# Performance work log

Measured on AMD Instinct MI355X. Metric: run time of the kernel, lower is better.

## Reference

```python
import jax, jax.numpy as jnp
import numpy as np

H = 16  # num_heads
D = 64  # head_dim (latent_dim // num_heads)


def setup_inputs() -> dict:
    key = jax.random.key(0)
    ks = jax.random.split(key, 14)
    B, L, S = 2, 1024, 4096
    input_dim, latent_dim, latent_rank = 2048, 1024, 128
    sc = 0.02
    return {
        "latent": jax.random.normal(ks[0], (B, L, latent_dim), jnp.float32),
        "x": jax.random.normal(ks[1], (B, S, input_dim), jnp.float32),
        "Wq": jax.random.normal(ks[2], (latent_dim, latent_dim), jnp.float32) * sc,
        "bq": jnp.zeros((latent_dim,), jnp.float32),
        "Wc": jax.random.normal(ks[3], (input_dim, latent_rank), jnp.float32) * sc,
        "bc": jnp.zeros((latent_rank,), jnp.float32),
        "Wk": jax.random.normal(ks[4], (latent_rank, latent_dim), jnp.float32) * sc,
        "bk": jnp.zeros((latent_dim,), jnp.float32),
        "Wv": jax.random.normal(ks[5], (latent_rank, latent_dim), jnp.float32) * sc,
        "bv": jnp.zeros((latent_dim,), jnp.float32),
        "Wo": jax.random.normal(ks[6], (latent_dim, latent_dim), jnp.float32) * sc,
        "bo": jnp.zeros((latent_dim,), jnp.float32),
    }


def reference(latent, x, Wq, bq, Wc, bc, Wk, bk, Wv, bv, Wo, bo):
    B, L, latent_dim = latent.shape
    S = x.shape[1]
    # projections
    Q = latent @ Wq + bq                      # [B, L, latent_dim]
    compressed = x @ Wc + bc                  # [B, S, latent_rank] low-rank latent
    K_full = compressed @ Wk + bk             # [B, S, latent_dim]
    V_full = compressed @ Wv + bv             # [B, S, latent_dim]
    # split heads -> [B, H, len, D]
    Qh = Q.reshape(B, L, H, D).transpose(0, 2, 1, 3)
    Kh = K_full.reshape(B, S, H, D).transpose(0, 2, 1, 3)
    Vh = V_full.reshape(B, S, H, D).transpose(0, 2, 1, 3)
    scale = 1.0 / jnp.sqrt(jnp.float32(D))
    scores = jnp.einsum("bhld,bhsd->bhls", Qh, Kh) * scale  # [B,H,L,S]
    attn = jax.nn.softmax(scores, axis=-1)
    ctx = jnp.einsum("bhls,bhsd->bhld", attn, Vh)            # [B,H,L,D]
    ctx = ctx.transpose(0, 2, 1, 3).reshape(B, L, latent_dim)
    return ctx @ Wo + bo
```

## Files before the change

### kernel.cpp

```cpp
#include <hip/hip_runtime.h>
#include <hip/hip_bf16.h>

using bf16x8  = __attribute__((ext_vector_type(8))) short;
using ushort8 = __attribute__((ext_vector_type(8))) unsigned short;
using f32x4   = __attribute__((ext_vector_type(4))) float;

#define DEVINL __device__ __forceinline__

DEVINL unsigned short f2bf(float f) {
    unsigned u = __builtin_bit_cast(unsigned, f);
    u += 0x7FFFu + ((u >> 16) & 1u);
    return (unsigned short)(u >> 16);
}

DEVINL void gload_lds16(const void* g, void* l) {
    __builtin_amdgcn_global_load_lds(
        (const __attribute__((address_space(1))) void*)g,
        (__attribute__((address_space(3))) void*)l, 16, 0, 0);
}

__global__ __launch_bounds__(256) void k_convT(const float* __restrict__ i0,
                                               unsigned short* __restrict__ o0,
                                               const float* __restrict__ i1,
                                               unsigned short* __restrict__ o1,
                                               int R, int C) {
    __shared__ float t[32][33];
    const float* in = blockIdx.z ? i1 : i0;
    unsigned short* out = blockIdx.z ? o1 : o0;
    int c0 = blockIdx.x * 32, r0 = blockIdx.y * 32;
    int tx = threadIdx.x, ty = threadIdx.y;
#pragma unroll
    for (int i = 0; i < 4; i++)
        t[ty + i * 8][tx] = in[(size_t)(r0 + ty + i * 8) * C + c0 + tx];
    __syncthreads();
#pragma unroll
    for (int i = 0; i < 4; i++)
        out[(size_t)(c0 + ty + i * 8) * R + r0 + tx] = f2bf(t[tx][ty + i * 8]);
}

template <int BM, int BN, int OUTBF, int BIASROW, int AMODE>
__global__ __launch_bounds__(256) void k_gemm(const void* __restrict__ Ain,
                                              const unsigned short* __restrict__ BT,
                                              const float* __restrict__ bias,
                                              void* __restrict__ Cout,
                                              int M, int N, int K, float scale,
                                              size_t zA, size_t zB, size_t zC,
                                              const float2* __restrict__ ML) {
    constexpr int WM = BM / 2, WN = BN / 2, MI = WM / 16, NI = WN / 16;
    constexpr int CB = BN * 8 / 256;
    constexpr int CA = BM * 8 / 256;
    constexpr int EPT = BM * 64 / 256;
    constexpr int TPR = 64 / EPT;
    constexpr int NAREG = (AMODE == 2) ? EPT / 2 : (AMODE == 1 ? EPT / 4 : 1);
    __shared__ unsigned short ls[2][(BM + BN) * 64];
    const int tid = threadIdx.x, lane = tid & 63, w = tid >> 6;
    const int m0 = blockIdx.y * BM, n0 = blockIdx.x * BN, zz = blockIdx.z;
    const int mw = (w >> 1) * WM, nw = (w & 1) * WN;
    const int r16 = lane & 15, g4 = lane >> 4;
    const unsigned short* A16 = (const unsigned short*)Ain + zA * zz;
    const float* A32 = (const float*)Ain;
    BT += zB * zz;
    const int arow = tid / TPR, acol = (tid % TPR) * EPT;

    float4 areg[NAREG];
    float2 mle[2];

    f32x4 acc[MI][NI];
#pragma unroll
    for (int a = 0; a < MI; a++)
#pragma unroll
        for (int b = 0; b < NI; b++) acc[a][b] = (f32x4){0.f, 0.f, 0.f, 0.f};

    auto LOAD_A = [&](int bufi, int k0) {
        if constexpr (AMODE == 0) {
#pragma unroll
            for (int i = 0; i < CA; i++) {
                int ch = i * 256 + w * 64 + lane;
                int row = ch >> 3, c = ch & 7;
                gload_lds16(A16 + (size_t)(m0 + row) * K + k0 + c * 8,
                            &ls[bufi][(size_t)(i * 256 + w * 64) * 8]);
            }
        } else if constexpr (AMODE == 1) {
            const float* src = A32 + (size_t)(m0 + arow) * K + k0 + acol;
#pragma unroll
            for (int j = 0; j < EPT / 4; j++) areg[j] = *(const float4*)(src + j * 4);
        } else {
            const float* src = A32 + (size_t)(m0 + arow) * K + k0 + acol;
#pragma unroll
            for (int j = 0; j < EPT / 4; j++) {
                areg[j] = *(const float4*)(src + j * 4);
                areg[j + EPT / 4] = *(const float4*)(src + 2097152 + j * 4);
            }
            int b = (m0 + arow) >> 10, q = (m0 + arow) & 1023, h = k0 >> 6;
            mle[0] = ML[((size_t)(b * 16 + h)) * 1024 + q];
            mle[1] = ML[((size_t)((2 + b) * 16 + h)) * 1024 + q];
        }
    };

    auto WRITE_A = [&](int bufi) {
        if constexpr (AMODE == 1) {
            unsigned u[EPT / 2];
#pragma unroll
            for (int j = 0; j < EPT / 4; j++) {
                asm("v_cvt_pk_bf16_f32 %0, %1, %2"
                    : "=v"(u[2 * j]) : "v"(areg[j].x), "v"(areg[j].y));
                asm("v_cvt_pk_bf16_f32 %0, %1, %2"
                    : "=v"(u[2 * j + 1]) : "v"(areg[j].z), "v"(areg[j].w));
            }
#pragma unroll
            for (int j = 0; j < EPT / 8; j++)
                *(uint4*)&ls[bufi][arow * 64 + acol + j * 8] =
                    make_uint4(u[4 * j], u[4 * j + 1], u[4 * j + 2], u[4 * j + 3]);
        } else if constexpr (AMODE == 2) {
            float Mx = fmaxf(mle[0].x, mle[1].x);
            float w0 = exp2f(mle[0].x - Mx), w1 = exp2f(mle[1].x - Mx);
            float inv = 1.f / (w0 * mle[0].y + w1 * mle[1].y);
            w0 *= inv; w1 *= inv;
            unsigned u[EPT / 2];
#pragma unroll
            for (int j = 0; j < EPT / 4; j++) {
                float4 a = areg[j], c = areg[j + EPT / 4];
                float v0 = w0 * a.x + w1 * c.x, v1 = w0 * a.y + w1 * c.y;
                float v2 = w0 * a.z + w1 * c.z, v3 = w0 * a.w + w1 * c.w;
                asm("v_cvt_pk_bf16_f32 %0, %1, %2" : "=v"(u[2 * j]) : "v"(v0), "v"(v1));
                asm("v_cvt_pk_bf16_f32 %0, %1, %2" : "=v"(u[2 * j + 1]) : "v"(v2), "v"(v3));
            }
#pragma unroll
            for (int j = 0; j < EPT / 8; j++)
                *(uint4*)&ls[bufi][arow * 64 + acol + j * 8] =
                    make_uint4(u[4 * j], u[4 * j + 1], u[4 * j + 2], u[4 * j + 3]);
        }
    };

    auto STAGE_B = [&](int bufi, int k0) {
        unsigned short* lsB = &ls[bufi][BM * 64];
#pragma unroll
        for (int i = 0; i < CB; i++) {
            int ch = i * 256 + w * 64 + lane;
            int row = ch >> 3, c = ch & 7;
            gload_lds16(BT + (size_t)(n0 + row) * K + k0 + c * 8,
                        lsB + (size_t)(i * 256 + w * 64) * 8);
        }
    };

    auto COMPUTE = [&](int bufi) {
        const unsigned short* lsA = ls[bufi];
        const unsigned short* lsB = &ls[bufi][BM * 64];
#pragma unroll
        for (int kk = 0; kk < 2; kk++) {
            bf16x8 af[MI], bfr[NI];
#pragma unroll
            for (int a = 0; a < MI; a++)
                af[a] = *(const bf16x8*)&lsA[(mw + a * 16 + r16) * 64 + kk * 32 + g4 * 8];
#pragma unroll
            for (int b = 0; b < NI; b++)
                bfr[b] = *(const bf16x8*)&lsB[(nw + b * 16 + r16) * 64 + kk * 32 + g4 * 8];
#pragma unroll
            for (int a = 0; a < MI; a++)
#pragma unroll
                for (int b = 0; b < NI; b++)
                    acc[a][b] = __builtin_amdgcn_mfma_f32_16x16x32_bf16(af[a], bfr[b], acc[a][b], 0, 0, 0);
        }
    };

    const int nk = K >> 6;
    LOAD_A(0, 0);
    STAGE_B(0, 0);
    if constexpr (AMODE != 0) WRITE_A(0);
    __syncthreads();
    for (int t = 0; t < nk; ++t) {
        int cur = t & 1, nxt = cur ^ 1;
        if (t + 1 < nk) { LOAD_A(nxt, (t + 1) << 6); STAGE_B(nxt, (t + 1) << 6); }
        COMPUTE(cur);
        if (AMODE != 0 && t + 1 < nk) WRITE_A(nxt);
        __syncthreads();
    }

#pragma unroll
    for (int b = 0; b < NI; b++) {
        int col = n0 + nw + b * 16 + r16;
        float bvc = BIASROW ? 0.f : bias[col];
#pragma unroll
        for (int a = 0; a < MI; a++) {
#pragma unroll
            for (int r = 0; r < 4; r++) {
                int row = m0 + mw + a * 16 + g4 * 4 + r;
                float bv = BIASROW ? bias[row] : bvc;
                float v = (acc[a][b][r] + bv) * scale;
                if (OUTBF)
                    ((unsigned short*)Cout)[zC * zz + (size_t)row * N + col] = f2bf(v);
                else
                    ((float*)Cout)[zC * zz + (size_t)row * N + col] = v;
            }
        }
    }
}

__global__ __launch_bounds__(256, 4) void k_attn(const unsigned short* __restrict__ Qb,
                                                 const unsigned short* __restrict__ Kb,
                                                 const unsigned short* __restrict__ VTb,
                                                 float* __restrict__ ctxp,
                                                 float2* __restrict__ ML) {
    constexpr int LD = 1024;
    __shared__ unsigned short lsK[2][64 * 64];
    __shared__ unsigned short lsVT[2][64 * 64];
    __shared__ unsigned short lsP[4][16 * 64];
    const int tid = threadIdx.x, lane = tid & 63, w = tid >> 6;
    const int r16 = lane & 15, g4 = lane >> 4;
    const int wg = blockIdx.x;
    const int xcd = wg & 7, t_ = wg >> 3, qi = t_ & 15, gg = t_ >> 4;
    const int g = gg * 8 + xcd;
    const int bh = g & 31, z = g >> 5;
    const int b = bh >> 4, h = bh & 15;
    const int q0 = qi * 64 + w * 16;

    const size_t qbase = ((size_t)b * 1024 + q0 + r16) * LD + h * 64;
    bf16x8 qa0 = *(const bf16x8*)&Qb[qbase + g4 * 8];
    bf16x8 qa1 = *(const bf16x8*)&Qb[qbase + 32 + g4 * 8];

    f32x4 ctxa[4];
#pragma unroll
    for (int d = 0; d < 4; d++) ctxa[d] = (f32x4){0.f, 0.f, 0.f, 0.f};
    float m_run = -1e30f, l_run = 0.f;

    const int s7 = r16 & 7;
    const int offk0 = r16 * 64 + ((g4 ^ s7) << 3);
    const int offk1 = r16 * 64 + (((g4 + 4) ^ s7) << 3);
    const int pwb = r16 * 64 + (g4 & 1) * 4;
    const int c2 = g4 >> 1;
    const int swn0 = ((0 + c2) ^ s7) << 3, swn1 = ((2 + c2) ^ s7) << 3;
    const int swn2 = ((4 + c2) ^ s7) << 3, swn3 = ((6 + c2) ^ s7) << 3;

    const int lrow = lane >> 3, lcol = lane & 7;
    const int csrc = lcol ^ lrow;
    const unsigned short* gK = Kb + (size_t)b * 4096 * LD + h * 64 +
                               (size_t)(w * 8 + lrow) * LD + csrc * 8;
    const unsigned short* gV = VTb + (size_t)bh * 64 * 4096 +
                               (size_t)(w * 8 + lrow) * 4096 + csrc * 8;

    auto STAGE = [&](int bufi, int s0) {
        gload_lds16(gK + (size_t)s0 * LD, &lsK[bufi][(w * 8) * 64]);
        gload_lds16(gK + (size_t)(s0 + 32) * LD, &lsK[bufi][(32 + w * 8) * 64]);
        gload_lds16(gV + s0, &lsVT[bufi][(w * 8) * 64]);
        gload_lds16(gV + s0 + 32 * 4096, &lsVT[bufi][(32 + w * 8) * 64]);
    };

    auto COMPUTE = [&](int bufi) {
        f32x4 sc[4];
#pragma unroll
        for (int ni = 0; ni < 4; ni++) sc[ni] = (f32x4){0.f, 0.f, 0.f, 0.f};
        __builtin_amdgcn_s_setprio(1);
#pragma unroll
        for (int kk = 0; kk < 2; kk++) {
            bf16x8 qa = kk ? qa1 : qa0;
            int ofk = kk ? offk1 : offk0;
#pragma unroll
            for (int ni = 0; ni < 4; ni++) {
                bf16x8 kf = *(const bf16x8*)&lsK[bufi][ni * 1024 + ofk];
                sc[ni] = __builtin_amdgcn_mfma_f32_16x16x32_bf16(kf, qa, sc[ni], 0, 0, 0);
            }
        }
        __builtin_amdgcn_s_setprio(0);

        float pmax = sc[0][0];
#pragma unroll
        for (int ni = 0; ni < 4; ni++)
#pragma unroll
            for (int r = 0; r < 4; r++)
                if (ni || r) pmax = fmaxf(pmax, sc[ni][r]);
        pmax = fmaxf(pmax, __shfl_xor(pmax, 16));
        pmax = fmaxf(pmax, __shfl_xor(pmax, 32));

        if (!__all(pmax <= m_run + 8.f)) {
            float mn = fmaxf(m_run, pmax);
            float corr = exp2f(m_run - mn);
            m_run = mn;
            l_run *= corr;
            float c4[4];
#pragma unroll
            for (int r = 0; r < 4; r++) c4[r] = __shfl(corr, g4 * 4 + r);
#pragma unroll
            for (int di = 0; di < 4; di++)
#pragma unroll
                for (int r = 0; r < 4; r++) ctxa[di][r] *= c4[r];
        }

        float p[4][4];
        float rs = 0.f;
#pragma unroll
        for (int ni = 0; ni < 4; ni++)
#pragma unroll
            for (int r = 0; r < 4; r++) {
                p[ni][r] = exp2f(sc[ni][r] - m_run);
                rs += p[ni][r];
            }
        rs += __shfl_xor(rs, 16);
        rs += __shfl_xor(rs, 32);
        l_run += rs;

#pragma unroll
        for (int ni = 0; ni < 4; ni++) {
            int sw = ni == 0 ? swn0 : ni == 1 ? swn1 : ni == 2 ? swn2 : swn3;
            unsigned u0, u1;
            asm("v_cvt_pk_bf16_f32 %0, %1, %2" : "=v"(u0) : "v"(p[ni][0]), "v"(p[ni][1]));
            asm("v_cvt_pk_bf16_f32 %0, %1, %2" : "=v"(u1) : "v"(p[ni][2]), "v"(p[ni][3]));
            *(uint2*)&lsP[w][pwb + sw] = make_uint2(u0, u1);
        }

        __builtin_amdgcn_s_setprio(1);
#pragma unroll
        for (int kk = 0; kk < 2; kk++) {
            int ofk = kk ? offk1 : offk0;
            bf16x8 pa = *(const bf16x8*)&lsP[w][ofk];
#pragma unroll
            for (int di = 0; di < 4; di++) {
                bf16x8 vf = *(const bf16x8*)&lsVT[bufi][di * 1024 + ofk];
                ctxa[di] = __builtin_amdgcn_mfma_f32_16x16x32_bf16(pa, vf, ctxa[di], 0, 0, 0);
            }
        }
        __builtin_amdgcn_s_setprio(0);
    };

    const int t0 = z * 32, t1 = t0 + 32;
    STAGE(0, t0 * 64);
    __syncthreads();
#pragma unroll 1
    for (int t = t0; t < t1; ++t) {
        int pb = (t - t0) & 1;
        if (t + 1 < t1) STAGE(pb ^ 1, (t + 1) * 64);
        COMPUTE(pb);
        __syncthreads();
    }

    float* cp = ctxp + ((size_t)z * 2 + b) * 1024 * 1024;
#pragma unroll
    for (int r = 0; r < 4; r++) {
        int q = q0 + g4 * 4 + r;
#pragma unroll
        for (int di = 0; di < 4; di++)
            cp[(size_t)q * 1024 + h * 64 + di * 16 + r16] = ctxa[di][r];
    }
    if (g4 == 0)
        ML[(((size_t)z * 2 + b) * 16 + h) * 1024 + q0 + r16] = make_float2(m_run, l_run);
}

extern "C" void kernel_launch(void* const* d_in, const int* in_sizes, int n_in,
                              void* d_out, int out_size, void* d_ws, size_t ws_size,
                              hipStream_t stream) {
    const float* latent = (const float*)d_in[0];
    const float* x      = (const float*)d_in[1];
    const float* Wq     = (const float*)d_in[2];
    const float* bq     = (const float*)d_in[3];
    const float* Wc     = (const float*)d_in[4];
    const float* bc     = (const float*)d_in[5];
    const float* Wk     = (const float*)d_in[6];
    const float* bk     = (const float*)d_in[7];
    const float* Wv     = (const float*)d_in[8];
    const float* bv     = (const float*)d_in[9];
    const float* Wo     = (const float*)d_in[10];
    const float* bo     = (const float*)d_in[11];
    float* out = (float*)d_out;

    char* ws = (char*)d_ws;
    size_t off = 0;
    auto alloc = [&](size_t shorts) {
        void* p = ws + off;
        off += (shorts * 2 + 255) & ~(size_t)255;
        return (unsigned short*)p;
    };
    unsigned short* WqT  = alloc(1048576);
    unsigned short* WcT  = alloc(262144);
    unsigned short* WkT  = alloc(131072);
    unsigned short* WvT  = alloc(131072);
    unsigned short* WoT  = alloc(1048576);
    unsigned short* comp = alloc(1048576);
    unsigned short* Qb   = alloc(2097152);
    unsigned short* Kb   = alloc(8388608);
    unsigned short* VTb  = alloc(8388608);
    float*          ctxp = (float*)alloc(8388608);
    float2*         MLp  = (float2*)alloc(262144);

    dim3 tb(32, 8);
    k_convT<<<dim3(32, 32, 2), tb, 0, stream>>>(Wq, WqT, Wo, WoT, 1024, 1024);
    k_convT<<<dim3(32, 4, 2), tb, 0, stream>>>(Wk, WkT, Wv, WvT, 128, 1024);
    k_convT<<<dim3(4, 64, 1), tb, 0, stream>>>(Wc, WcT, Wc, WcT, 2048, 128);

    k_gemm<32, 128, 1, 0, 1><<<dim3(1, 256, 1), 256, 0, stream>>>(
        x, WcT, bc, comp, 8192, 128, 2048, 1.f, 0, 0, 0, nullptr);
    k_gemm<64, 64, 1, 0, 1><<<dim3(16, 32, 1), 256, 0, stream>>>(
        latent, WqT, bq, Qb, 2048, 1024, 1024, 0.18033688f, 0, 0, 0, nullptr);
    k_gemm<128, 128, 1, 0, 0><<<dim3(8, 64, 1), 256, 0, stream>>>(
        comp, WkT, bk, Kb, 8192, 1024, 128, 1.f, 0, 0, 0, nullptr);
    k_gemm<64, 64, 1, 1, 0><<<dim3(64, 16, 2), 256, 0, stream>>>(
        WvT, comp, bv, VTb, 1024, 4096, 128, 1.f,
        0, (size_t)4096 * 128, (size_t)16 * 64 * 4096, nullptr);
    k_attn<<<1024, 256, 0, stream>>>(Qb, Kb, VTb, ctxp, MLp);
    k_gemm<64, 64, 0, 0, 2><<<dim3(16, 32, 1), 256, 0, stream>>>(
        ctxp, WoT, bo, out, 2048, 1024, 1024, 1.f, 0, 0, 0, MLp);
}
```

Measured before the change: 300.5 us.

## Software-pipeline attention PV with next QK, merge transposes, retile GEMMs

The attention loop is restructured so the PV MFMAs for the previous tile run after the QK MFMAs of the current tile, with V fragments preloaded into registers. This overlaps softmax latency with matrix work, and the row-sum reduction across lanes is deferred to the end. Separately, the three weight-transpose launches are merged into one kernel, and the compress and K projection GEMMs switch to 64x64 tiles for more blocks. The pipelining raises register pressure through the extra V fragment registers, which could lower occupancy.

```diff
diff --git a/kernel.cpp b/kernel.cpp
--- a/kernel.cpp
+++ b/kernel.cpp
@@ -19,15 +19,23 @@
         (__attribute__((address_space(3))) void*)l, 16, 0, 0);
 }
 
-__global__ __launch_bounds__(256) void k_convT(const float* __restrict__ i0,
-                                               unsigned short* __restrict__ o0,
-                                               const float* __restrict__ i1,
-                                               unsigned short* __restrict__ o1,
-                                               int R, int C) {
+__global__ __launch_bounds__(256) void k_convTall(
+        const float* __restrict__ Wq, const float* __restrict__ Wo,
+        const float* __restrict__ Wk, const float* __restrict__ Wv,
+        const float* __restrict__ Wc,
+        unsigned short* __restrict__ WqT, unsigned short* __restrict__ WoT,
+        unsigned short* __restrict__ WkT, unsigned short* __restrict__ WvT,
+        unsigned short* __restrict__ WcT) {
     __shared__ float t[32][33];
-    const float* in = blockIdx.z ? i1 : i0;
-    unsigned short* out = blockIdx.z ? o1 : o0;
-    int c0 = blockIdx.x * 32, r0 = blockIdx.y * 32;
+    int bx = blockIdx.x;
+    const float* in; unsigned short* out; int R, C, tix;
+    if (bx < 1024)      { in = Wq; out = WqT; R = 1024; C = 1024; tix = bx; }
+    else if (bx < 2048) { in = Wo; out = WoT; R = 1024; C = 1024; tix = bx - 1024; }
+    else if (bx < 2176) { in = Wk; out = WkT; R = 128;  C = 1024; tix = bx - 2048; }
+    else if (bx < 2304) { in = Wv; out = WvT; R = 128;  C = 1024; tix = bx - 2176; }
+    else                { in = Wc; out = WcT; R = 2048; C = 128;  tix = bx - 2304; }
+    int ctiles = C >> 5;
+    int c0 = (tix % ctiles) * 32, r0 = (tix / ctiles) * 32;
     int tx = threadIdx.x, ty = threadIdx.y;
 #pragma unroll
     for (int i = 0; i < 4; i++)
@@ -228,8 +236,8 @@
     const int offk1 = r16 * 64 + (((g4 + 4) ^ s7) << 3);
     const int pwb = r16 * 64 + (g4 & 1) * 4;
     const int c2 = g4 >> 1;
-    const int swn0 = ((0 + c2) ^ s7) << 3, swn1 = ((2 + c2) ^ s7) << 3;
-    const int swn2 = ((4 + c2) ^ s7) << 3, swn3 = ((6 + c2) ^ s7) << 3;
+    const int swn[4] = {((0 + c2) ^ s7) << 3, ((2 + c2) ^ s7) << 3,
+                        ((4 + c2) ^ s7) << 3, ((6 + c2) ^ s7) << 3};
 
     const int lrow = lane >> 3, lcol = lane & 7;
     const int csrc = lcol ^ lrow;
@@ -238,6 +246,8 @@
     const unsigned short* gV = VTb + (size_t)bh * 64 * 4096 +
                                (size_t)(w * 8 + lrow) * 4096 + csrc * 8;
 
+    bf16x8 vfr[8];
+
     auto STAGE = [&](int bufi, int s0) {
         gload_lds16(gK + (size_t)s0 * LD, &lsK[bufi][(w * 8) * 64]);
         gload_lds16(gK + (size_t)(s0 + 32) * LD, &lsK[bufi][(32 + w * 8) * 64]);
@@ -245,10 +255,7 @@
         gload_lds16(gV + s0 + 32 * 4096, &lsVT[bufi][(32 + w * 8) * 64]);
     };
 
-    auto COMPUTE = [&](int bufi) {
-        f32x4 sc[4];
-#pragma unroll
-        for (int ni = 0; ni < 4; ni++) sc[ni] = (f32x4){0.f, 0.f, 0.f, 0.f};
+    auto QK = [&](int bufi, f32x4* sc) {
         __builtin_amdgcn_s_setprio(1);
 #pragma unroll
         for (int kk = 0; kk < 2; kk++) {
@@ -261,16 +268,28 @@
             }
         }
         __builtin_amdgcn_s_setprio(0);
-
-        float pmax = sc[0][0];
-#pragma unroll
-        for (int ni = 0; ni < 4; ni++)
-#pragma unroll
-            for (int r = 0; r < 4; r++)
-                if (ni || r) pmax = fmaxf(pmax, sc[ni][r]);
+    };
+
+    auto PV = [&](bf16x8 pa0, bf16x8 pa1) {
+        __builtin_amdgcn_s_setprio(1);
+#pragma unroll
+        for (int kk = 0; kk < 2; kk++) {
+            bf16x8 pa = kk ? pa1 : pa0;
+#pragma unroll
+            for (int di = 0; di < 4; di++)
+                ctxa[di] = __builtin_amdgcn_mfma_f32_16x16x32_bf16(pa, vfr[kk * 4 + di], ctxa[di], 0, 0, 0);
+        }
+        __builtin_amdgcn_s_setprio(0);
+    };
+
+    auto SOFTMAX = [&](f32x4* sc) {
+        float pmax = fmaxf(fmaxf(fmaxf(sc[0][0], sc[0][1]), fmaxf(sc[0][2], sc[0][3])),
+                           fmaxf(fmaxf(sc[1][0], sc[1][1]), fmaxf(sc[1][2], sc[1][3])));
+        pmax = fmaxf(pmax,
+               fmaxf(fmaxf(fmaxf(sc[2][0], sc[2][1]), fmaxf(sc[2][2], sc[2][3])),
+                     fmaxf(fmaxf(sc[3][0], sc[3][1]), fmaxf(sc[3][2], sc[3][3]))));
         pmax = fmaxf(pmax, __shfl_xor(pmax, 16));
         pmax = fmaxf(pmax, __shfl_xor(pmax, 32));
-
         if (!__all(pmax <= m_run + 8.f)) {
             float mn = fmaxf(m_run, pmax);
             float corr = exp2f(m_run - mn);
@@ -284,53 +303,68 @@
 #pragma unroll
                 for (int r = 0; r < 4; r++) ctxa[di][r] *= c4[r];
         }
-
         float p[4][4];
-        float rs = 0.f;
 #pragma unroll
         for (int ni = 0; ni < 4; ni++)
 #pragma unroll
             for (int r = 0; r < 4; r++) {
                 p[ni][r] = exp2f(sc[ni][r] - m_run);
-                rs += p[ni][r];
-            }
-        rs += __shfl_xor(rs, 16);
-        rs += __shfl_xor(rs, 32);
-        l_run += rs;
-
+                l_run += p[ni][r];
+            }
 #pragma unroll
         for (int ni = 0; ni < 4; ni++) {
-            int sw = ni == 0 ? swn0 : ni == 1 ? swn1 : ni == 2 ? swn2 : swn3;
             unsigned u0, u1;
             asm("v_cvt_pk_bf16_f32 %0, %1, %2" : "=v"(u0) : "v"(p[ni][0]), "v"(p[ni][1]));
             asm("v_cvt_pk_bf16_f32 %0, %1, %2" : "=v"(u1) : "v"(p[ni][2]), "v"(p[ni][3]));
-            *(uint2*)&lsP[w][pwb + sw] = make_uint2(u0, u1);
-        }
-
-        __builtin_amdgcn_s_setprio(1);
+            *(uint2*)&lsP[w][pwb + swn[ni]] = make_uint2(u0, u1);
+        }
+    };
+
+    auto LOADVF = [&](int bufi) {
 #pragma unroll
         for (int kk = 0; kk < 2; kk++) {
             int ofk = kk ? offk1 : offk0;
-            bf16x8 pa = *(const bf16x8*)&lsP[w][ofk];
-#pragma unroll
-            for (int di = 0; di < 4; di++) {
-                bf16x8 vf = *(const bf16x8*)&lsVT[bufi][di * 1024 + ofk];
-                ctxa[di] = __builtin_amdgcn_mfma_f32_16x16x32_bf16(pa, vf, ctxa[di], 0, 0, 0);
-            }
-        }
-        __builtin_amdgcn_s_setprio(0);
+#pragma unroll
+            for (int di = 0; di < 4; di++)
+                vfr[kk * 4 + di] = *(const bf16x8*)&lsVT[bufi][di * 1024 + ofk];
+        }
     };
 
     const int t0 = z * 32, t1 = t0 + 32;
     STAGE(0, t0 * 64);
     __syncthreads();
+    {
+        STAGE(1, (t0 + 1) * 64);
+        f32x4 sc[4];
+#pragma unroll
+        for (int ni = 0; ni < 4; ni++) sc[ni] = (f32x4){0.f, 0.f, 0.f, 0.f};
+        QK(0, sc);
+        SOFTMAX(sc);
+        LOADVF(0);
+        __syncthreads();
+    }
 #pragma unroll 1
-    for (int t = t0; t < t1; ++t) {
-        int pb = (t - t0) & 1;
-        if (t + 1 < t1) STAGE(pb ^ 1, (t + 1) * 64);
-        COMPUTE(pb);
+    for (int t = t0 + 1; t < t1; ++t) {
+        int cur = (t - t0) & 1;
+        bf16x8 pa0 = *(const bf16x8*)&lsP[w][offk0];
+        bf16x8 pa1 = *(const bf16x8*)&lsP[w][offk1];
+        if (t + 1 < t1) STAGE(cur ^ 1, (t + 1) * 64);
+        f32x4 sc[4];
+#pragma unroll
+        for (int ni = 0; ni < 4; ni++) sc[ni] = (f32x4){0.f, 0.f, 0.f, 0.f};
+        QK(cur, sc);
+        PV(pa0, pa1);
+        SOFTMAX(sc);
+        LOADVF(cur);
         __syncthreads();
     }
+    {
+        bf16x8 pa0 = *(const bf16x8*)&lsP[w][offk0];
+        bf16x8 pa1 = *(const bf16x8*)&lsP[w][offk1];
+        PV(pa0, pa1);
+    }
+    l_run += __shfl_xor(l_run, 16);
+    l_run += __shfl_xor(l_run, 32);
 
     float* cp = ctxp + ((size_t)z * 2 + b) * 1024 * 1024;
 #pragma unroll
@@ -380,16 +414,13 @@
     float*          ctxp = (float*)alloc(8388608);
     float2*         MLp  = (float2*)alloc(262144);
 
-    dim3 tb(32, 8);
-    k_convT<<<dim3(32, 32, 2), tb, 0, stream>>>(Wq, WqT, Wo, WoT, 1024, 1024);
-    k_convT<<<dim3(32, 4, 2), tb, 0, stream>>>(Wk, WkT, Wv, WvT, 128, 1024);
-    k_convT<<<dim3(4, 64, 1), tb, 0, stream>>>(Wc, WcT, Wc, WcT, 2048, 128);
-
-    k_gemm<32, 128, 1, 0, 1><<<dim3(1, 256, 1), 256, 0, stream>>>(
+    k_convTall<<<2560, dim3(32, 8), 0, stream>>>(Wq, Wo, Wk, Wv, Wc,
+                                                 WqT, WoT, WkT, WvT, WcT);
+    k_gemm<64, 64, 1, 0, 1><<<dim3(2, 128, 1), 256, 0, stream>>>(
         x, WcT, bc, comp, 8192, 128, 2048, 1.f, 0, 0, 0, nullptr);
     k_gemm<64, 64, 1, 0, 1><<<dim3(16, 32, 1), 256, 0, stream>>>(
         latent, WqT, bq, Qb, 2048, 1024, 1024, 0.18033688f, 0, 0, 0, nullptr);
-    k_gemm<128, 128, 1, 0, 0><<<dim3(8, 64, 1), 256, 0, stream>>>(
+    k_gemm<64, 64, 1, 0, 0><<<dim3(16, 128, 1), 256, 0, stream>>>(
         comp, WkT, bk, Kb, 8192, 1024, 128, 1.f, 0, 0, 0, nullptr);
     k_gemm<64, 64, 1, 1, 0><<<dim3(64, 16, 2), 256, 0, stream>>>(
         WvT, comp, bv, VTb, 1024, 4096, 128, 1.f,
```

Measured after the change: 300.3 us. No clear change (-0.1%).
